# Performance work log

Measured on AMD Instinct MI355X. Metric: run time of the kernel, lower is better.

## Reference

```python
import jax, jax.numpy as jnp
import numpy as np

K = 16
EPS = 1e-5
SLOPE = 0.2


def knn_idx(k, xyz_k, xyz_q):
    # xyz_k: (B,Nk,3), xyz_q: (B,Nq,3) -> (B,Nq,k) indices of k nearest in xyz_k
    d = (jnp.sum(xyz_q * xyz_q, -1, keepdims=True)
         - 2.0 * jnp.einsum('bqc,bkc->bqk', xyz_q, xyz_k)
         + jnp.sum(xyz_k * xyz_k, -1)[:, None, :])
    _, idx = jax.lax.top_k(-d, k)
    return idx


def graph_feature(coor_q, x_q, coor_k, x_k):
    # coor_*: (B,N*,3); x_q: (B,C,Nq); x_k: (B,C,Nk) -> (B,2C,Nq,K)
    idx = knn_idx(K, coor_k, coor_q)                      # (B,Nq,K)
    nbr = jax.vmap(lambda xk, i: xk[:, i])(x_k, idx)       # (B,C,Nq,K)
    xq = x_q[:, :, :, None]                                # (B,C,Nq,1)
    xq = jnp.broadcast_to(xq, nbr.shape)
    return jnp.concatenate([nbr - xq, xq], axis=1)


def group_norm(x, gamma, beta, groups=4):
    B, C, N, Kk = x.shape
    xg = x.reshape(B, groups, C // groups, N, Kk)
    mu = jnp.mean(xg, axis=(2, 3, 4), keepdims=True)
    var = jnp.var(xg, axis=(2, 3, 4), keepdims=True)
    xn = ((xg - mu) / jnp.sqrt(var + EPS)).reshape(B, C, N, Kk)
    return xn * gamma[None, :, None, None] + beta[None, :, None, None]


def cgl(f, W, gamma, beta):
    # 1x1 Conv2d (no bias) + GroupNorm(4) + LeakyReLU(0.2)
    y = jnp.einsum('oc,bcnk->bonk', W, f)
    return jax.nn.leaky_relu(group_norm(y, gamma, beta), SLOPE)


def fps(xyz, m):
    # furthest point sampling. xyz: (B,N,3) -> (B,m) int32
    B, N, _ = xyz.shape
    first = jnp.zeros((B,), jnp.int32)

    def body(carry, _):
        dist, last = carry
        lp = jnp.take_along_axis(xyz, last[:, None, None].astype(jnp.int32), axis=1)  # (B,1,3)
        d = jnp.sum((xyz - lp) ** 2, -1)
        dist = jnp.minimum(dist, d)
        nxt = jnp.argmax(dist, -1).astype(jnp.int32)
        return (dist, nxt), nxt

    init = (jnp.full((B, N), 1e10, jnp.float32), first)
    _, rest = jax.lax.scan(body, init, None, length=m - 1)  # (m-1,B)
    return jnp.concatenate([first[None, :], rest], axis=0).T  # (B,m)


def fps_downsample(coor, x, m):
    # coor: (B,N,3), x: (B,C,N) -> new_coor (B,3,m), new_x (B,C,m)
    idx = fps(coor, m)                                        # (B,m)
    new_coor = jnp.take_along_axis(coor, idx[:, :, None], axis=1).transpose(0, 2, 1)
    new_x = jnp.take_along_axis(x, idx[:, None, :], axis=2)
    return new_coor, new_x


def setup_inputs() -> dict:
    key = jax.random.key(0)
    ks = jax.random.split(key, 16)
    d = {
        'x': jax.random.normal(ks[0], (8, 4096, 3), jnp.float32),
        'num0': 2048, 'num1': 512, 'num2': 128,
        'w_in': jax.random.normal(ks[1], (8, 3), jnp.float32) * 0.3,
        'b_in': jnp.zeros((8,), jnp.float32),
    }
    layer_dims = {'1': (32, 16), '2': (64, 64), '4': (128, 128),
                  '5': (128, 256), '6': (256, 256), '7': (256, 512)}
    for i, (name, (o, c)) in enumerate(layer_dims.items()):
        d[f'w{name}'] = jax.random.normal(ks[2 + i], (o, c), jnp.float32) * (1.0 / np.sqrt(c))
        d[f'g{name}'] = jnp.ones((o,), jnp.float32)
        d[f'be{name}'] = jnp.zeros((o,), jnp.float32)
    return d


def reference(x, num0, num1, num2, w_in, b_in,
              w1, g1, be1, w2, g2, be2, w4, g4, be4,
              w5, g5, be5, w6, g6, be6, w7, g7, be7):
    xyz = x.transpose(0, 2, 1)                                # (B,3,N)
    coor = x                                                  # (B,N,3)
    f = jnp.einsum('oc,bcn->bon', w_in, xyz) + b_in[None, :, None]  # (B,8,N)

    f = cgl(graph_feature(coor, f, coor, f), w1, g1, be1)     # (B,32,N,K)
    f = jnp.max(f, axis=-1)                                   # (B,32,N)

    sp1, f_q = fps_downsample(coor, f, num0)                  # (B,3,n0),(B,32,n0)
    coor_d = sp1.transpose(0, 2, 1)                           # (B,n0,3)
    f = cgl(graph_feature(coor_d, f_q, coor, f), w2, g2, be2)
    stage1_feature = jnp.max(f, axis=-1)                      # (B,64,n0)
    coor = coor_d

    sp2, f_q = fps_downsample(coor, stage1_feature, num1)
    coor_d = sp2.transpose(0, 2, 1)
    f = cgl(graph_feature(coor_d, f_q, coor, stage1_feature), w4, g4, be4)
    f = jnp.max(f, axis=-1)                                   # (B,128,n1)
    f = cgl(graph_feature(coor_d, f, coor_d, f), w5, g5, be5)
    stage2_feature = jnp.max(f, axis=-1)                      # (B,128,n1)
    coor = coor_d

    sp3, f_q = fps_downsample(coor, stage2_feature, num2)
    coor_d = sp3.transpose(0, 2, 1)
    f = cgl(graph_feature(coor_d, f_q, coor, stage2_feature), w6, g6, be6)
    f = jnp.max(f, axis=-1)                                   # (B,256,n2)
    f = cgl(graph_feature(coor_d, f, coor_d, f), w7, g7, be7)
    stage3_feature = jnp.max(f, axis=-1)                      # (B,256,n2)

    out_coor = sp3.transpose(0, 2, 1)                         # (B,n2,3)
    out_f = stage3_feature.transpose(0, 2, 1)                 # (B,n2,256)
    return out_coor, out_f
```

## Files before the change

### kernel.cpp

```cpp
#include <hip/hip_runtime.h>
#include <hip/hip_bf16.h>
#include <math.h>

#define DEVI __device__ __forceinline__
typedef unsigned long long ull;
typedef float f32x2 __attribute__((ext_vector_type(2)));

__global__ void k_feat0(const float* __restrict__ x,
                        const float* __restrict__ w_in,
                        const float* __restrict__ b_in,
                        float* __restrict__ coords0, float* __restrict__ feat0,
                        float* __restrict__ stats)
{
  int t = blockIdx.x*blockDim.x + threadIdx.x;
  if (t < 384) stats[t] = 0.f;
  if (t >= 8*4096) return;
  float cx = x[t*3+0], cy = x[t*3+1], cz = x[t*3+2];
  coords0[t*3+0]=cx; coords0[t*3+1]=cy; coords0[t*3+2]=cz;
  #pragma unroll
  for (int o=0;o<8;o++){
    float s = __fadd_rn(__fadd_rn(__fmul_rn(cx,w_in[o*3+0]),
                                  __fmul_rn(cy,w_in[o*3+1])),
                        __fmul_rn(cz,w_in[o*3+2]));
    feat0[t*8+o] = __fadd_rn(s, b_in[o]);
  }
}

DEVI f32x2 pk_sub(f32x2 a, f32x2 b){
  f32x2 r;
  asm("v_pk_add_f32 %0, %1, %2 neg_lo:[0,1] neg_hi:[0,1]" : "=v"(r) : "v"(a), "v"(b));
  return r;
}
DEVI f32x2 pk_mul(f32x2 a, f32x2 b){
  f32x2 r; asm("v_pk_mul_f32 %0, %1, %2" : "=v"(r) : "v"(a), "v"(b)); return r;
}
DEVI f32x2 pk_add(f32x2 a, f32x2 b){
  f32x2 r; asm("v_pk_add_f32 %0, %1, %2" : "=v"(r) : "v"(a), "v"(b)); return r;
}

template<int CTRL>
DEVI float dppmaxf(float x){
  float o = __int_as_float(__builtin_amdgcn_update_dpp(__float_as_int(x),__float_as_int(x),CTRL,0xF,0xF,false));
  return fmaxf(x,o);
}
template<int CTRL>
DEVI unsigned dppminu(unsigned x){
  unsigned o = (unsigned)__builtin_amdgcn_update_dpp((int)x,(int)x,CTRL,0xF,0xF,false);
  return (x < o) ? x : o;
}

template<int P>
DEVI void fps_stage(f32x2 (&px)[P/2], f32x2 (&py)[P/2], f32x2 (&pz)[P/2],
                    int m, float sx, float sy, float sz,
                    const float* cpx, const float* cpy, const float* cpz,
                    ull* mK,
                    int* ssel, float* snx, float* sny, float* snz, int tid)
{
  const int wv = tid>>6, lane = tid&63;
  float dist[P];
  #pragma unroll
  for (int p=0;p<P;p++) dist[p]=1e10f;
  if (tid==0){ ssel[0]=0; if (snx){ snx[0]=sx; sny[0]=sy; snz[0]=sz; } }
  #pragma unroll 1
  for (int it=1; it<m; it++){
    f32x2 vsx, vsy, vsz;
    vsx.x=sx; vsx.y=sx; vsy.x=sy; vsy.y=sy; vsz.x=sz; vsz.y=sz;
    float bv = -1.f;
    #pragma unroll
    for (int i=0;i<P/2;i++){
      f32x2 dx = pk_sub(px[i], vsx);
      f32x2 dy = pk_sub(py[i], vsy);
      f32x2 dz = pk_sub(pz[i], vsz);
      f32x2 s  = pk_add(pk_add(pk_mul(dx,dx), pk_mul(dy,dy)), pk_mul(dz,dz));
      float d0 = fminf(dist[2*i],   s.x);
      float d1 = fminf(dist[2*i+1], s.y);
      dist[2*i] = d0; dist[2*i+1] = d1;
      bv = fmaxf(bv, d0);
      bv = fmaxf(bv, d1);
    }
    int bidx = 0;
    #pragma unroll
    for (int p=P-1;p>=0;p--) if (dist[p]==bv) bidx = tid+(p<<8);
    float w = bv;
    w = dppmaxf<0x111>(w);
    w = dppmaxf<0x112>(w);
    w = dppmaxf<0x114>(w);
    w = dppmaxf<0x118>(w);
    w = dppmaxf<0x142>(w);
    w = dppmaxf<0x143>(w);
    float bvw = __uint_as_float((unsigned)__builtin_amdgcn_readlane(__float_as_int(w),63));
    unsigned cand = (bv == bvw) ? (unsigned)bidx : 0xFFFFFFFFu;
    cand = dppminu<0x111>(cand);
    cand = dppminu<0x112>(cand);
    cand = dppminu<0x114>(cand);
    cand = dppminu<0x118>(cand);
    cand = dppminu<0x142>(cand);
    cand = dppminu<0x143>(cand);
    const unsigned itu = (unsigned)it;
    ull* slot = mK + ((it&1)<<2);
    if (lane==63){
      unsigned lo = ((~cand & 0xFFFu)<<12) | itu;
      *(volatile ull*)(slot + wv) = ((ull)__float_as_uint(bvw)<<32) | (ull)lo;
    }
    ull k0,k1,k2,k3;
    for (;;){
      asm volatile("" ::: "memory");
      k0=slot[0]; k1=slot[1]; k2=slot[2]; k3=slot[3];
      unsigned chk = (((unsigned)k0 ^ itu) | ((unsigned)k1 ^ itu) |
                      ((unsigned)k2 ^ itu) | ((unsigned)k3 ^ itu)) & 0xFFFu;
      if (chk == 0u) break;
    }
    ull ka = (k1>k0)?k1:k0;
    ull kb = (k3>k2)?k3:k2;
    ull kw = (kb>ka)?kb:ka;
    int gi = (int)((~((unsigned)(kw & 0xffffffffull) >> 12)) & 0xFFFu);
    sx = cpx[gi]; sy = cpy[gi]; sz = cpz[gi];
    if (tid==0){
      ssel[it]=gi;
      if (snx){ snx[it]=sx; sny[it]=sy; snz[it]=sz; }
    }
  }
}

template<int CTRL>
DEVI void dppmin_fj(float& d, int& j){
  float od = __int_as_float(__builtin_amdgcn_update_dpp(__float_as_int(d),__float_as_int(d),CTRL,0xF,0xF,false));
  int   oj = __builtin_amdgcn_update_dpp(j,j,CTRL,0xF,0xF,false);
  bool tk = (od < d) || (od == d && oj < j);
  d = tk?od:d; j = tk?oj:j;
}

DEVI float dist_qk(const float* __restrict__ ckb, int j,
                   float qx, float qy, float qz, float sqq){
  float kx=ckb[3*j], ky=ckb[3*j+1], kz=ckb[3*j+2];
  float sk  = __fadd_rn(__fadd_rn(__fmul_rn(kx,kx),__fmul_rn(ky,ky)),
                        __fmul_rn(kz,kz));
  float dot = __fadd_rn(__fadd_rn(__fmul_rn(qx,kx),__fmul_rn(qy,ky)),
                        __fmul_rn(qz,kz));
  return __fadd_rn(__fsub_rn(sqq, __fmul_rn(2.0f,dot)), sk);
}

template<int NPL>
DEVI void knn_wave(const float* __restrict__ cq, int Nq,
                   const float* __restrict__ ck, int Nk,
                   int* __restrict__ idx_out, int b, int q, int lane)
{
  size_t r3 = ((size_t)b*Nq+q)*3;
  float qx=cq[r3], qy=cq[r3+1], qz=cq[r3+2];
  float sqq = __fadd_rn(__fadd_rn(__fmul_rn(qx,qx),__fmul_rn(qy,qy)),
                        __fmul_rn(qz,qz));
  constexpr int GS = (NPL < 8) ? NPL : 8;
  constexpr int NG = NPL / GS;
  float gv[NG]; int gj[NG];
  const float* ckb = ck + (size_t)b*Nk*3;
  ull exmask = 0;
  int dirtyg = -1;
  int myout = 0;
  #pragma unroll 1
  for (int r=0; r<16; r++){
    #pragma unroll
    for (int g=0; g<NG; g++){
      if (dirtyg < 0 || dirtyg == g){
        float nv=__int_as_float(0x7f800000); int nj=0x7fffffff;
        #pragma unroll
        for (int e=0; e<GS; e++){
          const int i = g*GS+e;
          int j = lane + (i<<6);
          float d = dist_qk(ckb, j, qx,qy,qz, sqq);
          bool rem = ((exmask >> i) & 1ull) == 0ull;
          if (rem && d < nv){ nv=d; nj=j; }
        }
        gv[g]=nv; gj[g]=nj;
      }
    }
    float lv = gv[0]; int lj = gj[0];
    #pragma unroll
    for (int g=1; g<NG; g++)
      if (gv[g]<lv || (gv[g]==lv && gj[g]<lj)){ lv=gv[g]; lj=gj[g]; }
    float rd = lv; int rj = lj;
    dppmin_fj<0x111>(rd,rj);
    dppmin_fj<0x112>(rd,rj);
    dppmin_fj<0x114>(rd,rj);
    dppmin_fj<0x118>(rd,rj);
    dppmin_fj<0x142>(rd,rj);
    dppmin_fj<0x143>(rd,rj);
    int wj = __builtin_amdgcn_readlane(rj,63);
    if (lane == r) myout = wj;
    if ((wj & 63) == lane) exmask |= (1ull << (wj>>6));
    dirtyg = (wj>>6)/GS;
  }
  if (lane<16) idx_out[((size_t)b*Nq+q)*16 + lane] = myout;
}

template<int NPL>
__global__ __launch_bounds__(256,3) void k_knn_t(const float* __restrict__ cq, int Nq,
                                                 const float* __restrict__ ck, int Nk,
                                                 int* __restrict__ idx_out)
{
  const int b = blockIdx.y;
  const int q = blockIdx.x*4 + (threadIdx.x>>6);
  if (q >= Nq) return;
  knn_wave<NPL>(cq, Nq, ck, Nk, idx_out, b, q, threadIdx.x&63);
}

__global__ __launch_bounds__(256) void k_fps_knn1(
    const float* __restrict__ coords0,
    int* __restrict__ idx1, int* __restrict__ idx2, int* __restrict__ idx3,
    float* __restrict__ c1, float* __restrict__ c2, float* __restrict__ c3,
    float* __restrict__ out, int* __restrict__ knn1)
{
  __shared__ float s1x[4096], s1y[4096], s1z[4096];
  __shared__ float s2x[2048], s2y[2048], s2z[2048];
  __shared__ float s3x[512],  s3y[512],  s3z[512];
  __shared__ float s4x[128],  s4y[128],  s4z[128];
  __shared__ int   ssel[2048];
  __shared__ alignas(32) ull mK[8];
  if (blockIdx.x >= 8){
    int flat = blockIdx.x - 8;
    int b = flat >> 10, qb = flat & 1023;
    int q = qb*4 + (threadIdx.x>>6);
    knn_wave<64>(coords0, 4096, coords0, 4096, knn1, b, q, threadIdx.x&63);
    return;
  }
  const int b = blockIdx.x, tid = threadIdx.x;
  __builtin_amdgcn_s_setprio(3);
  const float* cb = coords0 + (size_t)b*4096*3;
  if (tid<8) mK[tid] = ~0ull;
  {
    f32x2 px[8], py[8], pz[8];
    #pragma unroll
    for (int i=0;i<8;i++){
      int j0 = tid + ((2*i)<<8), j1 = tid + ((2*i+1)<<8);
      float X0=cb[3*j0], Y0=cb[3*j0+1], Z0=cb[3*j0+2];
      float X1=cb[3*j1], Y1=cb[3*j1+1], Z1=cb[3*j1+2];
      px[i].x=X0; px[i].y=X1; py[i].x=Y0; py[i].y=Y1; pz[i].x=Z0; pz[i].y=Z1;
      s1x[j0]=X0; s1y[j0]=Y0; s1z[j0]=Z0;
      s1x[j1]=X1; s1y[j1]=Y1; s1z[j1]=Z1;
    }
    float sx=cb[0], sy=cb[1], sz=cb[2];
    __syncthreads();
    fps_stage<16>(px,py,pz, 2048, sx,sy,sz, s1x,s1y,s1z,
                  mK, ssel, s2x,s2y,s2z, tid);
  }
  __syncthreads();
  {
    float* c1b = c1 + (size_t)b*2048*3;
    for (int i=tid;i<2048;i+=256){
      idx1[b*2048+i]=ssel[i];
      c1b[3*i]=s2x[i]; c1b[3*i+1]=s2y[i]; c1b[3*i+2]=s2z[i];
    }
  }
  {
    f32x2 px[4], py[4], pz[4];
    #pragma unroll
    for (int i=0;i<4;i++){
      int j0 = tid + ((2*i)<<8), j1 = tid + ((2*i+1)<<8);
      px[i].x=s2x[j0]; px[i].y=s2x[j1];
      py[i].x=s2y[j0]; py[i].y=s2y[j1];
      pz[i].x=s2z[j0]; pz[i].y=s2z[j1];
    }
    float sx=s2x[0], sy=s2y[0], sz=s2z[0];
    __syncthreads();
    fps_stage<8>(px,py,pz, 512, sx,sy,sz, s2x,s2y,s2z,
                 mK, ssel, s3x,s3y,s3z, tid);
  }
  __syncthreads();
  {
    float* c2b = c2 + (size_t)b*512*3;
    for (int i=tid;i<512;i+=256){
      idx2[b*512+i]=ssel[i];
      c2b[3*i]=s3x[i]; c2b[3*i+1]=s3y[i]; c2b[3*i+2]=s3z[i];
    }
  }
  {
    f32x2 px[1], py[1], pz[1];
    {
      int j0 = tid, j1 = tid + 256;
      px[0].x=s3x[j0]; px[0].y=s3x[j1];
      py[0].x=s3y[j0]; py[0].y=s3y[j1];
      pz[0].x=s3z[j0]; pz[0].y=s3z[j1];
    }
    float sx=s3x[0], sy=s3y[0], sz=s3z[0];
    __syncthreads();
    fps_stage<2>(px,py,pz, 128, sx,sy,sz, s3x,s3y,s3z,
                 mK, ssel, s4x,s4y,s4z, tid);
  }
  __syncthreads();
  {
    float* c3b = c3 + (size_t)b*128*3;
    float* ob  = out + (size_t)b*128*3;
    for (int i=tid;i<128;i+=256){
      idx3[b*128+i]=ssel[i];
      float X=s4x[i],Y=s4y[i],Z=s4z[i];
      c3b[3*i]=X; c3b[3*i+1]=Y; c3b[3*i+2]=Z;
      ob[3*i]=X; ob[3*i+1]=Y; ob[3*i+2]=Z;
    }
  }
}

struct WtParams {
  const float* W[6];
  float* wl[6];
  float* wq[6];
  int O[6], C[6], OC[6];
};
__global__ void k_wt_all(WtParams p){
  int s = blockIdx.y;
  int t = blockIdx.x*blockDim.x + threadIdx.x;
  int OC = p.OC[s];
  if (t >= OC) return;
  int C = p.C[s], O = p.O[s];
  int o = t / C, c = t - o*C;
  const float* W = p.W[s];
  float wlv = W[o*2*C + c];
  float wrv = W[o*2*C + C + c];
  p.wl[s][c*O+o] = wlv;
  p.wq[s][c*O+o] = wrv - wlv;
}

#define GEMM_M 8
__global__ void k_gemm_dual(const float* __restrict__ feat, int Nk, int C, int O,
                            const float* __restrict__ wlT, const float* __restrict__ wqT,
                            float* __restrict__ yk, float* __restrict__ yq)
{
  extern __shared__ float sf[];
  const int b = blockIdx.y;
  const int o = threadIdx.x & (O-1);
  const int rg = threadIdx.x / O;
  const int R = blockDim.x / O;
  const int rowsPB = R*GEMM_M;
  const int row0 = blockIdx.x * rowsPB;
  const int Cp = C+1;
  const float* src = feat + ((size_t)b*Nk + row0)*C;
  for (int i=threadIdx.x; i<rowsPB*C; i+=blockDim.x){
    int r = i / C, c = i - r*C;
    sf[r*Cp + c] = src[i];
  }
  __syncthreads();
  float ak[GEMM_M], aq[GEMM_M];
  #pragma unroll
  for (int m=0;m<GEMM_M;m++){ ak[m]=0.f; aq[m]=0.f; }
  const float* lp = wlT + o;
  const float* qp = wqT + o;
  const float* sfr = sf + rg*GEMM_M*Cp;
  for (int c=0;c<C;c++){
    float wl = lp[(size_t)c*O];
    float wq = qp[(size_t)c*O];
    #pragma unroll
    for (int m=0;m<GEMM_M;m++){
      float xv = sfr[m*Cp + c];
      ak[m] = fmaf(xv, wl, ak[m]);
      aq[m] = fmaf(xv, wq, aq[m]);
    }
  }
  size_t obase = ((size_t)b*Nk + row0 + rg*GEMM_M)*O + o;
  #pragma unroll
  for (int m=0;m<GEMM_M;m++){
    yk[obase + (size_t)m*O] = ak[m];
    yq[obase + (size_t)m*O] = aq[m];
  }
}

__global__ void k_gather(const float* __restrict__ yk, const float* __restrict__ yq,
                         const int* __restrict__ knnidx, const int* __restrict__ qmap,
                         int Nq, int Nk, int O,
                         float* __restrict__ vmax, float* __restrict__ stats)
{
  const int b = blockIdx.y;
  const int o = threadIdx.x & (O-1);
  const int rg = threadIdx.x / O;
  const int R = blockDim.x / O;
  float ls=0.f, ls2=0.f;
  const float* ykb = yk + (size_t)b*Nk*O;
  const float* yqb = yq + (size_t)b*Nk*O;
  for (int nq = blockIdx.x*R + rg; nq < Nq; nq += gridDim.x*R){
    int qj = qmap ? qmap[b*Nq+nq] : nq;
    float vq = yqb[(size_t)qj*O + o];
    const int* ip = knnidx + ((size_t)b*Nq+nq)*16;
    float vmx = -3.4e38f;
    #pragma unroll
    for (int k=0;k<16;k++){
      int j = ip[k];
      float v = ykb[(size_t)j*O+o] + vq;
      vmx = fmaxf(vmx, v);
      ls += v; ls2 = fmaf(v,v,ls2);
    }
    vmax[((size_t)b*Nq+nq)*O+o] = vmx;
  }
  int span = O/4; if (span>64) span=64;
  for (int mm=1; mm<span; mm<<=1){
    ls  += __shfl_xor(ls, mm);
    ls2 += __shfl_xor(ls2, mm);
  }
  __shared__ float sred[8];
  if (threadIdx.x<8) sred[threadIdx.x]=0.f;
  __syncthreads();
  int lane = threadIdx.x & 63;
  if ((lane & (span-1))==0){
    int g = (o*4)/O;
    atomicAdd(&sred[g*2+0], ls);
    atomicAdd(&sred[g*2+1], ls2);
  }
  __syncthreads();
  if (threadIdx.x<8) atomicAdd(&stats[b*8+threadIdx.x], sred[threadIdx.x]);
}

__global__ void k_norm(const float* __restrict__ vmax, const float* __restrict__ stats,
                       const float* __restrict__ gamma,
                       const float* __restrict__ beta,
                       int Nq, int O, float invcnt, float* __restrict__ outf)
{
  const int b = blockIdx.y;
  const int n = Nq*O;
  for (int i = blockIdx.x*blockDim.x+threadIdx.x; i<n; i+=gridDim.x*blockDim.x){
    int o = i & (O-1);
    int g = (o*4)/O;
    float s1 = stats[b*8+g*2], s2 = stats[b*8+g*2+1];
    float mu = s1*invcnt;
    float var = fmaf(-mu,mu, s2*invcnt);
    float rs = 1.0f/sqrtf(var+1e-5f);
    float v = (vmax[(size_t)b*n + i]-mu)*rs*gamma[o] + beta[o];
    outf[(size_t)b*n + i] = (v>=0.f)? v : 0.2f*v;
  }
}

extern "C" void kernel_launch(void* const* d_in, const int* in_sizes, int n_in,
                              void* d_out, int out_size, void* d_ws, size_t ws_size,
                              hipStream_t stream)
{
  const int B = 8;
  const float* x    = (const float*)d_in[0];
  const float* w_in = (const float*)d_in[4];
  const float* b_in = (const float*)d_in[5];
  const float *Wm[6], *Gm[6], *Bm[6];
  for (int i=0;i<6;i++){
    Wm[i]=(const float*)d_in[6+3*i];
    Gm[i]=(const float*)d_in[6+3*i+1];
    Bm[i]=(const float*)d_in[6+3*i+2];
  }
  float* ws = (float*)d_ws;
  float* out = (float*)d_out;
  const size_t OFF_C0=0,        OFF_F0=98304,   OFF_F1=360448,  OFF_F2=1409024,
               OFF_F4=2457600,  OFF_F5=2981888, OFF_F6=3506176, OFF_F7=3768320,
               OFF_C1=4030464,  OFF_C2=4079616, OFF_C3=4091904,
               OFF_YK=4094976,  OFF_YQ=6192128, OFF_VM=8289280,
               OFF_WL=9337856,  OFF_WQ=9468928, OFF_ST=9600000,
               OFF_I1=9600384,  OFF_I2=9616768, OFF_I3=9620864, OFF_KNN=9621888,
               TOTAL=10146176;
  if (ws_size < TOTAL*sizeof(float)) return;
  float *c0=ws+OFF_C0, *f0=ws+OFF_F0, *f1=ws+OFF_F1, *f2=ws+OFF_F2,
        *f4=ws+OFF_F4, *f5=ws+OFF_F5, *f6=ws+OFF_F6,
        *c1=ws+OFF_C1, *c2=ws+OFF_C2, *c3=ws+OFF_C3,
        *yk=ws+OFF_YK, *yq=ws+OFF_YQ, *vm=ws+OFF_VM, *stats=ws+OFF_ST;
  int *i1=(int*)(ws+OFF_I1), *i2=(int*)(ws+OFF_I2), *i3=(int*)(ws+OFF_I3),
      *knn=(int*)(ws+OFF_KNN);

  const int OCs[6]  = {256, 2048, 8192, 16384, 32768, 65536};
  const int OCoff[6]= {0,   256,  2304, 10496, 26880, 59648};

  struct St { int C,O,Nk,Nq; const float* feat; const float* cq; const float* ck;
              const int* qmap; float* outf; };
  const St st[6] = {
    {8,   32, 4096, 4096, f0, c0, c0, nullptr, f1},
    {32,  64, 4096, 2048, f1, c1, c0, i1,      f2},
    {64, 128, 2048,  512, f2, c2, c1, i2,      f4},
    {128,128,  512,  512, f4, c2, c2, nullptr, f5},
    {128,256,  512,  128, f5, c3, c2, i3,      f6},
    {256,256,  128,  128, f6, c3, c3, nullptr, out + 8*128*3},
  };

  k_feat0 <<<(8*4096+255)/256, 256, 0, stream>>>(x, w_in, b_in, c0, f0, stats);

  WtParams wp;
  for (int s=0;s<6;s++){
    wp.W[s]=Wm[s];
    wp.wl[s]=ws+OFF_WL+OCoff[s];
    wp.wq[s]=ws+OFF_WQ+OCoff[s];
    wp.O[s]=st[s].O; wp.C[s]=st[s].C; wp.OC[s]=OCs[s];
  }
  k_wt_all<<<dim3(256,6), 256, 0, stream>>>(wp);

  k_fps_knn1<<<8 + 8*1024, 256, 0, stream>>>(c0, i1, i2, i3, c1, c2, c3,
                                             out, knn);

  for (int s=0;s<6;s++){
    const St& S = st[s];
    if (s > 0){
      dim3 gk((S.Nq + 3)/4, B);
      int npl = S.Nk >> 6;
      if      (npl == 64) k_knn_t<64><<<gk, 256, 0, stream>>>(S.cq, S.Nq, S.ck, S.Nk, knn);
      else if (npl == 32) k_knn_t<32><<<gk, 256, 0, stream>>>(S.cq, S.Nq, S.ck, S.Nk, knn);
      else if (npl ==  8) k_knn_t< 8><<<gk, 256, 0, stream>>>(S.cq, S.Nq, S.ck, S.Nk, knn);
      else                k_knn_t< 2><<<gk, 256, 0, stream>>>(S.cq, S.Nq, S.ck, S.Nk, knn);
    }
    int rowsPB = 2048 / S.O;
    dim3 gg(S.Nk / rowsPB, B);
    size_t shb = (size_t)rowsPB * (S.C+1) * sizeof(float);
    k_gemm_dual<<<gg, 256, shb, stream>>>(S.feat, S.Nk, S.C, S.O,
                                          ws+OFF_WL+OCoff[s], ws+OFF_WQ+OCoff[s],
                                          yk, yq);
    dim3 gs(64, B);
    k_gather<<<gs, 256, 0, stream>>>(yk, yq, knn, S.qmap, S.Nq, S.Nk, S.O,
                                     vm, stats + s*64);
    float invcnt = 1.0f / ((float)(S.O/4) * (float)S.Nq * 16.0f);
    dim3 gn((S.Nq*S.O + 255)/256, B);
    k_norm<<<gn, 256, 0, stream>>>(vm, stats + s*64, Gm[s], Bm[s],
                                   S.Nq, S.O, invcnt, S.outf);
  }
}
```

Before: 2.353 ms.

## Run later FPS stages on a single wavefront to avoid cross-wave sync

The second and third furthest-point-sampling stages now run on one 64-lane wavefront, with each lane holding 32 or 8 points. A DPP 64-bit max reduction (distance, inverted index) followed by a readlane replaces the multi-wave shared-memory slot handshake. This removes the per-iteration cross-wave synchronisation, which dominates cost on the small point sets. In exchange each lane does more serial distance work, and the other three waves sit idle during these stages.

```diff
diff --git a/kernel.cpp b/kernel.cpp
--- a/kernel.cpp
+++ b/kernel.cpp
@@ -47,6 +47,13 @@
 DEVI unsigned dppminu(unsigned x){
   unsigned o = (unsigned)__builtin_amdgcn_update_dpp((int)x,(int)x,CTRL,0xF,0xF,false);
   return (x < o) ? x : o;
+}
+template<int CTRL>
+DEVI void dppmax64(unsigned& hi, unsigned& lo){
+  unsigned oh = (unsigned)__builtin_amdgcn_update_dpp((int)hi,(int)hi,CTRL,0xF,0xF,false);
+  unsigned ol = (unsigned)__builtin_amdgcn_update_dpp((int)lo,(int)lo,CTRL,0xF,0xF,false);
+  bool tk = (oh > hi) || (oh == hi && ol > lo);
+  hi = tk?oh:hi; lo = tk?ol:lo;
 }
 
 template<int P>
@@ -122,6 +129,53 @@
   }
 }
 
+template<int P>
+DEVI void fps_stage_1w(f32x2 (&px)[P/2], f32x2 (&py)[P/2], f32x2 (&pz)[P/2],
+                       int m, float sx, float sy, float sz,
+                       const float* cpx, const float* cpy, const float* cpz,
+                       int* ssel, float* snx, float* sny, float* snz, int lane)
+{
+  float dist[P];
+  #pragma unroll
+  for (int p=0;p<P;p++) dist[p]=1e10f;
+  if (lane==0){ ssel[0]=0; snx[0]=sx; sny[0]=sy; snz[0]=sz; }
+  #pragma unroll 1
+  for (int it=1; it<m; it++){
+    f32x2 vsx, vsy, vsz;
+    vsx.x=sx; vsx.y=sx; vsy.x=sy; vsy.y=sy; vsz.x=sz; vsz.y=sz;
+    float bv = -1.f;
+    #pragma unroll
+    for (int i=0;i<P/2;i++){
+      f32x2 dx = pk_sub(px[i], vsx);
+      f32x2 dy = pk_sub(py[i], vsy);
+      f32x2 dz = pk_sub(pz[i], vsz);
+      f32x2 s  = pk_add(pk_add(pk_mul(dx,dx), pk_mul(dy,dy)), pk_mul(dz,dz));
+      float d0 = fminf(dist[2*i],   s.x);
+      float d1 = fminf(dist[2*i+1], s.y);
+      dist[2*i] = d0; dist[2*i+1] = d1;
+      bv = fmaxf(bv, d0);
+      bv = fmaxf(bv, d1);
+    }
+    int bidx = 0;
+    #pragma unroll
+    for (int p=P-1;p>=0;p--) if (dist[p]==bv) bidx = lane+(p<<6);
+    unsigned hi = __float_as_uint(bv);
+    unsigned lo = ~(unsigned)bidx;
+    dppmax64<0x111>(hi,lo);
+    dppmax64<0x112>(hi,lo);
+    dppmax64<0x114>(hi,lo);
+    dppmax64<0x118>(hi,lo);
+    dppmax64<0x142>(hi,lo);
+    dppmax64<0x143>(hi,lo);
+    int gi = (int)(~(unsigned)__builtin_amdgcn_readlane((int)lo,63));
+    sx = cpx[gi]; sy = cpy[gi]; sz = cpz[gi];
+    if (lane==0){
+      ssel[it]=gi;
+      snx[it]=sx; sny[it]=sy; snz[it]=sz;
+    }
+  }
+}
+
 template<int CTRL>
 DEVI void dppmin_fj(float& d, int& j){
   float od = __int_as_float(__builtin_amdgcn_update_dpp(__float_as_int(d),__float_as_int(d),CTRL,0xF,0xF,false));
@@ -250,19 +304,19 @@
       c1b[3*i]=s2x[i]; c1b[3*i+1]=s2y[i]; c1b[3*i+2]=s2z[i];
     }
   }
-  {
-    f32x2 px[4], py[4], pz[4];
-    #pragma unroll
-    for (int i=0;i<4;i++){
-      int j0 = tid + ((2*i)<<8), j1 = tid + ((2*i+1)<<8);
+  __syncthreads();
+  if (tid < 64){
+    f32x2 px[16], py[16], pz[16];
+    #pragma unroll
+    for (int i=0;i<16;i++){
+      int j0 = tid + ((2*i)<<6), j1 = tid + ((2*i+1)<<6);
       px[i].x=s2x[j0]; px[i].y=s2x[j1];
       py[i].x=s2y[j0]; py[i].y=s2y[j1];
       pz[i].x=s2z[j0]; pz[i].y=s2z[j1];
     }
     float sx=s2x[0], sy=s2y[0], sz=s2z[0];
-    __syncthreads();
-    fps_stage<8>(px,py,pz, 512, sx,sy,sz, s2x,s2y,s2z,
-                 mK, ssel, s3x,s3y,s3z, tid);
+    fps_stage_1w<32>(px,py,pz, 512, sx,sy,sz, s2x,s2y,s2z,
+                     ssel, s3x,s3y,s3z, tid);
   }
   __syncthreads();
   {
@@ -272,18 +326,19 @@
       c2b[3*i]=s3x[i]; c2b[3*i+1]=s3y[i]; c2b[3*i+2]=s3z[i];
     }
   }
-  {
-    f32x2 px[1], py[1], pz[1];
-    {
-      int j0 = tid, j1 = tid + 256;
-      px[0].x=s3x[j0]; px[0].y=s3x[j1];
-      py[0].x=s3y[j0]; py[0].y=s3y[j1];
-      pz[0].x=s3z[j0]; pz[0].y=s3z[j1];
+  __syncthreads();
+  if (tid < 64){
+    f32x2 px[4], py[4], pz[4];
+    #pragma unroll
+    for (int i=0;i<4;i++){
+      int j0 = tid + ((2*i)<<6), j1 = tid + ((2*i+1)<<6);
+      px[i].x=s3x[j0]; px[i].y=s3x[j1];
+      py[i].x=s3y[j0]; py[i].y=s3y[j1];
+      pz[i].x=s3z[j0]; pz[i].y=s3z[j1];
     }
     float sx=s3x[0], sy=s3y[0], sz=s3z[0];
-    __syncthreads();
-    fps_stage<2>(px,py,pz, 128, sx,sy,sz, s3x,s3y,s3z,
-                 mK, ssel, s4x,s4y,s4z, tid);
+    fps_stage_1w<8>(px,py,pz, 128, sx,sy,sz, s3x,s3y,s3z,
+                    ssel, s4x,s4y,s4z, tid);
   }
   __syncthreads();
   {
```

New measurement: 2.542 ms. +8.1%, slower.
